# Optimization experiments

Hardware: AMD Instinct MI355X
Metric: run time of the kernel (lower is better)

The kernel has to match this reference:

```python
import jax, jax.numpy as jnp
import numpy as np

N_NODES = 50000
N_EDGES = 1600000
SLOPE = 0.01  # LeakyReLU default negative slope


def _leaky(x):
    return jnp.where(x >= 0, x, SLOPE * x)


def _gcn(x, W, b, row, col, num_nodes):
    """PyG GCNConv: x' = D^{-1/2}(A+I)D^{-1/2} X W + b (self-loops already in row/col)."""
    x = x @ W  # [N, 64]
    deg = jax.ops.segment_sum(jnp.ones_like(row, dtype=x.dtype), col, num_segments=num_nodes)
    dinv = jnp.where(deg > 0, jax.lax.rsqrt(deg), 0.0)
    norm = dinv[row] * dinv[col]  # [E+N]
    msg = x[row] * norm[:, None]  # gather + scale, [E+N, 64]
    out = jax.ops.segment_sum(msg, col, num_segments=num_nodes)
    return out + b


def setup_inputs() -> dict:
    key = jax.random.key(0)
    ks = jax.random.split(key, 24)
    d = {}
    d["screen"] = jax.random.normal(ks[0], (N_NODES, 768), jnp.float32)
    d["des"] = jax.random.normal(ks[1], (N_NODES, 768), jnp.float32)
    d["tweet"] = jax.random.normal(ks[2], (N_NODES, 768), jnp.float32)
    d["profile"] = jax.random.normal(ks[3], (N_NODES, 5), jnp.float32)
    d["personal"] = jax.random.normal(ks[4], (N_NODES, 7), jnp.float32)
    d["edge"] = jax.random.randint(ks[5], (2, N_EDGES), 0, N_NODES, dtype=jnp.int32)

    def lin(k, fan_in, fan_out):
        s = 1.0 / np.sqrt(fan_in)
        k1, k2 = jax.random.split(k)
        W = jax.random.uniform(k1, (fan_in, fan_out), jnp.float32, -s, s)
        b = jax.random.uniform(k2, (fan_out,), jnp.float32, -s, s)
        return W, b

    d["W_screen"], d["b_screen"] = lin(ks[6], 768, 16)
    d["W_des"], d["b_des"] = lin(ks[7], 768, 16)
    d["W_tweet"], d["b_tweet"] = lin(ks[8], 768, 16)
    d["W_pro"], d["b_pro"] = lin(ks[9], 5, 8)
    d["W_per"], d["b_per"] = lin(ks[10], 7, 8)
    d["W_lin"], d["b_lin"] = lin(ks[11], 64, 64)
    d["W_g1"], d["b_g1"] = lin(ks[12], 64, 64)
    d["W_g2"], d["b_g2"] = lin(ks[13], 64, 64)
    d["W_g3"], d["b_g3"] = lin(ks[14], 64, 64)
    d["W_o1"], d["b_o1"] = lin(ks[15], 64, 64)
    d["W_o2"], d["b_o2"] = lin(ks[16], 64, 2)
    return d


def reference(screen, des, tweet, profile, personal, edge,
              W_screen, b_screen, W_des, b_des, W_tweet, b_tweet,
              W_pro, b_pro, W_per, b_per, W_lin, b_lin,
              W_g1, b_g1, W_g2, b_g2, W_g3, b_g3,
              W_o1, b_o1, W_o2, b_o2):
    n = screen.shape[0]
    # dropout layers act as identity in eval mode
    s = _leaky(screen @ W_screen + b_screen)
    de = _leaky(des @ W_des + b_des)
    t = _leaky(tweet @ W_tweet + b_tweet)
    p = _leaky(profile @ W_pro + b_pro)
    pe = _leaky(personal @ W_per + b_per)
    x1 = jnp.concatenate((s, de, t, p, pe), axis=1)  # [N, 64]
    x = _leaky(x1 @ W_lin + b_lin)
    # add self-loops once (shared by all three GCN layers)
    loops = jnp.arange(n, dtype=edge.dtype)
    row = jnp.concatenate([edge[0], loops])
    col = jnp.concatenate([edge[1], loops])
    x = _gcn(x, W_g1, b_g1, row, col, n) + x1
    x = _gcn(x, W_g2, b_g2, row, col, n) + x1
    x = _gcn(x, W_g3, b_g3, row, col, n) + x1
    x = _leaky(x @ W_o1 + b_o1)
    return jax.nn.sigmoid(x @ W_o2 + b_o2)
```

## Files before the change

### kernel.cpp

```cpp
#include <hip/hip_runtime.h>

__device__ __forceinline__ float leaky(float v) { return v >= 0.f ? v : 0.01f * v; }

__device__ __forceinline__ void fma4(float4& a, float s, const float4& w) {
    a.x = fmaf(s, w.x, a.x); a.y = fmaf(s, w.y, a.y);
    a.z = fmaf(s, w.z, a.z); a.w = fmaf(s, w.w, a.w);
}

__device__ __forceinline__ unsigned short f2bf(float x) {
    unsigned b = __float_as_uint(x);
    return (unsigned short)((b + 0x7FFFu + ((b >> 16) & 1u)) >> 16);
}
__device__ __forceinline__ float bf2f(unsigned short u) {
    return __uint_as_float(((unsigned)u) << 16);
}

typedef __attribute__((ext_vector_type(8))) short short8v;
typedef __attribute__((ext_vector_type(4))) float float4v;

__global__ __launch_bounds__(256) void k_scan_part(const int* __restrict__ deg,
                                                   int* __restrict__ part,
                                                   int* __restrict__ bsum, int N) {
    __shared__ int tmp[256];
    int tid = threadIdx.x;
    int i = blockIdx.x * 256 + tid;
    int v = (i < N) ? deg[i] : 0;
    tmp[tid] = v;
    __syncthreads();
    for (int ofs = 1; ofs < 256; ofs <<= 1) {
        int t = (tid >= ofs) ? tmp[tid - ofs] : 0;
        __syncthreads();
        tmp[tid] += t;
        __syncthreads();
    }
    int incl = tmp[tid];
    if (i < N) part[i] = incl - v;
    if (tid == 255) bsum[blockIdx.x] = incl;
}

__global__ __launch_bounds__(256) void k_scan_sums(const int* __restrict__ bsum,
                                                   int* __restrict__ boff, int NB,
                                                   int* __restrict__ offs_last) {
    __shared__ int tmp[256];
    int tid = threadIdx.x;
    int v = (tid < NB) ? bsum[tid] : 0;
    tmp[tid] = v;
    __syncthreads();
    for (int ofs = 1; ofs < 256; ofs <<= 1) {
        int t = (tid >= ofs) ? tmp[tid - ofs] : 0;
        __syncthreads();
        tmp[tid] += t;
        __syncthreads();
    }
    int incl = tmp[tid];
    if (tid < NB) boff[tid] = incl - v;
    if (tid == 255) offs_last[0] = incl;
}

__global__ __launch_bounds__(256) void k_scan_final(const int* __restrict__ part,
                                                    const int* __restrict__ boff,
                                                    const int* __restrict__ deg,
                                                    int* __restrict__ offs,
                                                    int* __restrict__ pos,
                                                    float* __restrict__ dinv, int N) {
    int i = blockIdx.x * 256 + threadIdx.x;
    if (i < N) {
        int o = part[i] + boff[blockIdx.x];
        offs[i] = o;
        pos[i] = o;
        dinv[i] = rsqrtf((float)(deg[i] + 1));
    }
}

__global__ __launch_bounds__(512) void k_featB(
    const float* __restrict__ s, const float* __restrict__ d, const float* __restrict__ t,
    const float* __restrict__ Ws, const float* __restrict__ bs2,
    const float* __restrict__ Wd, const float* __restrict__ bd2,
    const float* __restrict__ Wt, const float* __restrict__ bt2,
    const float* __restrict__ prof, const float* __restrict__ pers,
    const float* __restrict__ Wp, const float* __restrict__ bp,
    const float* __restrict__ Wpe, const float* __restrict__ bpe,
    const int* __restrict__ colv, int* __restrict__ deg, int E,
    float* __restrict__ x1g, int N, int NG, int NSM) {
    __shared__ short8v wfv[3072];

    const int bid = blockIdx.x;
    const int tid = threadIdx.x;

    {
        const int NW = 3 * NG + NSM;
        int eper = (E + NW - 1) / NW;
        int ebase = bid * eper;
        int eend = ebase + eper; if (eend > E) eend = E;
        for (int e = ebase + tid; e < eend; e += 512)
            atomicAdd(&deg[colv[e]], 1);
    }

    if (bid >= 3 * NG) {
        int n = (bid - 3 * NG) * 512 + tid;
        if (n >= N) return;
        float pv[5], pe[7];
#pragma unroll
        for (int i = 0; i < 5; ++i) pv[i] = prof[(size_t)n * 5 + i];
#pragma unroll
        for (int i = 0; i < 7; ++i) pe[i] = pers[(size_t)n * 7 + i];
        float o[16];
#pragma unroll
        for (int j = 0; j < 8; ++j) {
            float a = bp[j];
#pragma unroll
            for (int i = 0; i < 5; ++i) a = fmaf(pv[i], Wp[i * 8 + j], a);
            o[j] = leaky(a);
            float a2 = bpe[j];
#pragma unroll
            for (int i = 0; i < 7; ++i) a2 = fmaf(pe[i], Wpe[i * 8 + j], a2);
            o[8 + j] = leaky(a2);
        }
#pragma unroll
        for (int v = 0; v < 4; ++v)
            *reinterpret_cast<float4*>(x1g + (size_t)n * 64 + 48 + v * 4) =
                make_float4(o[v * 4], o[v * 4 + 1], o[v * 4 + 2], o[v * 4 + 3]);
        return;
    }

    const int f = bid / NG;
    const int grp = bid - f * NG;
    const float* __restrict__ X = (f == 0) ? s : ((f == 1) ? d : t);
    const float* __restrict__ W = (f == 0) ? Ws : ((f == 1) ? Wd : Wt);
    const float* __restrict__ B = (f == 0) ? bs2 : ((f == 1) ? bd2 : bt2);
    const int n0 = grp * 128;
    const int lane = tid & 63;
    const int wid = tid >> 6;

    short* wfs = (short*)wfv;
#pragma unroll
    for (int v = 0; v < 6; ++v) {
        int idx4 = tid + v * 512;
        float4 w4 = *reinterpret_cast<const float4*>(W + (size_t)idx4 * 4);
        int k = idx4 >> 2;
        int j0 = (idx4 & 3) * 4;
        int c = k >> 5, g = (k >> 3) & 3, i = k & 7;
        float wq[4] = {w4.x, w4.y, w4.z, w4.w};
#pragma unroll
        for (int q = 0; q < 4; ++q) {
            int sl = (c * 64 + g * 16 + j0 + q) * 8 + i;
            unsigned short h = f2bf(wq[q]);
            wfs[sl] = (short)h;
            wfs[12288 + sl] = (short)f2bf(wq[q] - bf2f(h));
        }
    }
    __syncthreads();

    const int nb = n0 + wid * 16;
    int mrow = nb + (lane & 15); if (mrow >= N) mrow = N - 1;
    const float* base = X + (size_t)mrow * 768 + ((lane >> 4) << 3);

    float4 pa[4], pb[4];
#pragma unroll
    for (int u = 0; u < 4; ++u) {
        pa[u] = *reinterpret_cast<const float4*>(base + u * 32);
        pb[u] = *reinterpret_cast<const float4*>(base + u * 32 + 4);
    }
    __builtin_amdgcn_sched_barrier(0);
    float4v acc = {0.f, 0.f, 0.f, 0.f};

#pragma unroll
    for (int c = 0; c < 24; ++c) {
        const int u = c & 3;
        float xs[8] = {pa[u].x, pa[u].y, pa[u].z, pa[u].w,
                       pb[u].x, pb[u].y, pb[u].z, pb[u].w};
        if (c + 4 < 24) {
            pa[u] = *reinterpret_cast<const float4*>(base + (c + 4) * 32);
            pb[u] = *reinterpret_cast<const float4*>(base + (c + 4) * 32 + 4);
        }
        short8v xh, xl;
#pragma unroll
        for (int i = 0; i < 8; ++i) {
            unsigned short h = f2bf(xs[i]);
            xh[i] = (short)h;
            xl[i] = (short)f2bf(xs[i] - bf2f(h));
        }
        short8v wh = wfv[c * 64 + lane];
        short8v wl = wfv[1536 + c * 64 + lane];
        acc = __builtin_amdgcn_mfma_f32_16x16x32_bf16(xh, wh, acc, 0, 0, 0);
        acc = __builtin_amdgcn_mfma_f32_16x16x32_bf16(xl, wh, acc, 0, 0, 0);
        acc = __builtin_amdgcn_mfma_f32_16x16x32_bf16(xh, wl, acc, 0, 0, 0);
        __builtin_amdgcn_sched_barrier(0);
    }

    int j = lane & 15;
    float bb = B[j];
#pragma unroll
    for (int r = 0; r < 4; ++r) {
        int n = nb + ((lane >> 4) << 2) + r;
        if (n < N) x1g[(size_t)n * 64 + f * 16 + j] = leaky(acc[r] + bb);
    }
}

__global__ __launch_bounds__(256) void k_lin1(const float* __restrict__ x1,
                                              const float* __restrict__ Wl,
                                              const float* __restrict__ bl,
                                              const float* __restrict__ Wg1,
                                              const float* __restrict__ dinvv,
                                              const int* __restrict__ rowv,
                                              const int* __restrict__ colv,
                                              int* __restrict__ pos,
                                              int* __restrict__ csr, int E,
                                              unsigned short* __restrict__ z,
                                              int N, int NGB) {
    __shared__ float4 xt4[1024];
    __shared__ float4 wt4[1024];
    const int tid = threadIdx.x;
    const int bid = blockIdx.x;

    {
        int eper = (E + NGB - 1) / NGB;
        int ebase = bid * eper;
        int eend = ebase + eper; if (eend > E) eend = E;
        int cols[8], rows[8];
#pragma unroll
        for (int r = 0; r < 8; ++r) {
            int e = ebase + tid + r * 256;
            cols[r] = (e < eend) ? colv[e] : -1;
            rows[r] = (e < eend) ? rowv[e] : 0;
        }
        int ps[8];
#pragma unroll
        for (int r = 0; r < 8; ++r)
            if (cols[r] >= 0) ps[r] = atomicAdd(&pos[cols[r]], 1);
#pragma unroll
        for (int r = 0; r < 8; ++r)
            if (cols[r] >= 0) csr[ps[r]] = rows[r];
    }

    const int n0 = bid * 64;
    const int nq = tid & 15;
    const int jq = tid >> 4;

#pragma unroll
    for (int v = 0; v < 4; ++v) {
        int L = v * 256 + tid;
        int n = L >> 4, c4 = L & 15;
        int nn = n0 + n; if (nn >= N) nn = N - 1;
        xt4[n * 16 + (c4 ^ (n & 15))] = *reinterpret_cast<const float4*>(x1 + (size_t)nn * 64 + c4 * 4);
        wt4[L] = *reinterpret_cast<const float4*>(Wl + (size_t)L * 4);
    }
    __syncthreads();

    float4 acc[4];
#pragma unroll
    for (int g = 0; g < 4; ++g) acc[g] = make_float4(0.f, 0.f, 0.f, 0.f);
    for (int k = 0; k < 64; k += 4) {
        float4 w0 = wt4[(k + 0) * 16 + jq];
        float4 w1 = wt4[(k + 1) * 16 + jq];
        float4 w2 = wt4[(k + 2) * 16 + jq];
        float4 w3 = wt4[(k + 3) * 16 + jq];
        int k4 = k >> 2;
#pragma unroll
        for (int g = 0; g < 4; ++g) {
            int n = nq + (g << 4);
            float4 xv = xt4[n * 16 + (k4 ^ (n & 15))];
            fma4(acc[g], xv.x, w0);
            fma4(acc[g], xv.y, w1);
            fma4(acc[g], xv.z, w2);
            fma4(acc[g], xv.w, w3);
        }
    }
    float4 bb = *reinterpret_cast<const float4*>(bl + jq * 4);
    __syncthreads();

#pragma unroll
    for (int g = 0; g < 4; ++g) {
        int n = nq + (g << 4);
        float4 h;
        h.x = leaky(acc[g].x + bb.x);
        h.y = leaky(acc[g].y + bb.y);
        h.z = leaky(acc[g].z + bb.z);
        h.w = leaky(acc[g].w + bb.w);
        xt4[n * 16 + (jq ^ (n & 15))] = h;
    }
#pragma unroll
    for (int v = 0; v < 4; ++v) {
        int L = v * 256 + tid;
        wt4[L] = *reinterpret_cast<const float4*>(Wg1 + (size_t)L * 4);
    }
    __syncthreads();

#pragma unroll
    for (int g = 0; g < 4; ++g) acc[g] = make_float4(0.f, 0.f, 0.f, 0.f);
    for (int k = 0; k < 64; k += 4) {
        float4 w0 = wt4[(k + 0) * 16 + jq];
        float4 w1 = wt4[(k + 1) * 16 + jq];
        float4 w2 = wt4[(k + 2) * 16 + jq];
        float4 w3 = wt4[(k + 3) * 16 + jq];
        int k4 = k >> 2;
#pragma unroll
        for (int g = 0; g < 4; ++g) {
            int n = nq + (g << 4);
            float4 xv = xt4[n * 16 + (k4 ^ (n & 15))];
            fma4(acc[g], xv.x, w0);
            fma4(acc[g], xv.y, w1);
            fma4(acc[g], xv.z, w2);
            fma4(acc[g], xv.w, w3);
        }
    }
#pragma unroll
    for (int g = 0; g < 4; ++g) {
        int n = nq + (g << 4);
        if (n0 + n >= N) continue;
        float dv = dinvv[n0 + n];
        ushort4 o;
        o.x = f2bf(acc[g].x * dv); o.y = f2bf(acc[g].y * dv);
        o.z = f2bf(acc[g].z * dv); o.w = f2bf(acc[g].w * dv);
        *reinterpret_cast<ushort4*>(z + (size_t)(n0 + n) * 64 + jq * 4) = o;
    }
}

__global__ __launch_bounds__(256, 4) void k_mm64(const float* __restrict__ xin,
                                                 const float* __restrict__ W,
                                                 const float* __restrict__ dinvv,
                                                 unsigned short* __restrict__ z, int N) {
    __shared__ float4 xt4[1024];
    __shared__ float4 wt4[1024];
    const int tid = threadIdx.x;
    const int n0 = blockIdx.x * 64;
#pragma unroll
    for (int v = 0; v < 4; ++v) {
        int L = v * 256 + tid;
        int n = L >> 4, c4 = L & 15;
        int nn = n0 + n; if (nn >= N) nn = N - 1;
        xt4[n * 16 + (c4 ^ (n & 15))] = *reinterpret_cast<const float4*>(xin + (size_t)nn * 64 + c4 * 4);
        wt4[L] = *reinterpret_cast<const float4*>(W + (size_t)L * 4);
    }
    __syncthreads();
    const int nq = tid & 15;
    const int jq = tid >> 4;
    float4 acc[4];
#pragma unroll
    for (int g = 0; g < 4; ++g) acc[g] = make_float4(0.f, 0.f, 0.f, 0.f);
    for (int k = 0; k < 64; k += 4) {
        float4 w0 = wt4[(k + 0) * 16 + jq];
        float4 w1 = wt4[(k + 1) * 16 + jq];
        float4 w2 = wt4[(k + 2) * 16 + jq];
        float4 w3 = wt4[(k + 3) * 16 + jq];
        int k4 = k >> 2;
#pragma unroll
        for (int g = 0; g < 4; ++g) {
            int n = nq + (g << 4);
            float4 xv = xt4[n * 16 + (k4 ^ (n & 15))];
            fma4(acc[g], xv.x, w0);
            fma4(acc[g], xv.y, w1);
            fma4(acc[g], xv.z, w2);
            fma4(acc[g], xv.w, w3);
        }
    }
#pragma unroll
    for (int g = 0; g < 4; ++g) {
        int n = nq + (g << 4);
        if (n0 + n >= N) continue;
        float dv = dinvv[n0 + n];
        ushort4 o;
        o.x = f2bf(acc[g].x * dv); o.y = f2bf(acc[g].y * dv);
        o.z = f2bf(acc[g].z * dv); o.w = f2bf(acc[g].w * dv);
        *reinterpret_cast<ushort4*>(z + (size_t)(n0 + n) * 64 + jq * 4) = o;
    }
}

__global__ __launch_bounds__(256) void k_agg(const unsigned short* __restrict__ z,
                                             const int* __restrict__ offs,
                                             const int* __restrict__ csr,
                                             const float* __restrict__ dinv,
                                             const float* __restrict__ bias,
                                             const float* __restrict__ x1,
                                             float* __restrict__ xout, int N) {
    int lane = threadIdx.x & 63;
    int c = blockIdx.x * 4 + (threadIdx.x >> 6);
    if (c >= N) return;
    int s = __builtin_amdgcn_readfirstlane(offs[c]);
    int e = __builtin_amdgcn_readfirstlane(offs[c + 1]);
    const int half = lane >> 5;
    const int d = lane & 31;
    const unsigned* __restrict__ zr = (const unsigned*)z;

    float ax = 0.f, ay = 0.f;
    if (half == 0) {
        unsigned sv = zr[(size_t)c * 32 + d];
        ax = bf2f((unsigned short)(sv & 0xffffu));
        ay = bf2f((unsigned short)(sv >> 16));
    }
    float ux[8] = {0, 0, 0, 0, 0, 0, 0, 0};
    float uy[8] = {0, 0, 0, 0, 0, 0, 0, 0};
    int j = s;
    for (; j + 16 <= e; j += 16) {
#pragma unroll
        for (int u = 0; u < 8; ++u) {
            int r0 = csr[j + 2 * u];
            int r1 = csr[j + 2 * u + 1];
            int r = half ? r1 : r0;
            unsigned v = zr[(size_t)r * 32 + d];
            ux[u] += bf2f((unsigned short)(v & 0xffffu));
            uy[u] += bf2f((unsigned short)(v >> 16));
        }
    }
    for (; j + 2 <= e; j += 2) {
        int r0 = csr[j];
        int r1 = csr[j + 1];
        int r = half ? r1 : r0;
        unsigned v = zr[(size_t)r * 32 + d];
        ax += bf2f((unsigned short)(v & 0xffffu));
        ay += bf2f((unsigned short)(v >> 16));
    }
    if (j < e && half == 0) {
        int r = csr[j];
        unsigned v = zr[(size_t)r * 32 + d];
        ax += bf2f((unsigned short)(v & 0xffffu));
        ay += bf2f((unsigned short)(v >> 16));
    }
    float tx = ax + ((ux[0] + ux[1]) + (ux[2] + ux[3])) + ((ux[4] + ux[5]) + (ux[6] + ux[7]));
    float ty = ay + ((uy[0] + uy[1]) + (uy[2] + uy[3])) + ((uy[4] + uy[5]) + (uy[6] + uy[7]));
    tx += __shfl_xor(tx, 32);
    ty += __shfl_xor(ty, 32);
    if (half == 0) {
        float dv = dinv[c];
        float2 bb = reinterpret_cast<const float2*>(bias)[d];
        float2 xx = *reinterpret_cast<const float2*>(x1 + (size_t)c * 64 + 2 * d);
        float2 o;
        o.x = dv * tx + bb.x + xx.x;
        o.y = dv * ty + bb.y + xx.y;
        *reinterpret_cast<float2*>(xout + (size_t)c * 64 + 2 * d) = o;
    }
}

__global__ __launch_bounds__(256) void k_head(const float* __restrict__ xin,
                                              const float* __restrict__ Wo1,
                                              const float* __restrict__ bo1,
                                              const float* __restrict__ Wo2,
                                              const float* __restrict__ bo2,
                                              float* __restrict__ out, int N) {
    __shared__ float xsg[64][65];
    __shared__ float wg[64][65];
    __shared__ float hs[64][65];
    __shared__ float wo2[128];
    const int tid = threadIdx.x;
    const int n0 = blockIdx.x * 64;
#pragma unroll
    for (int v = 0; v < 4; ++v) {
        int idx = tid + v * 256;
        int n = idx >> 4;
        int jj = (idx & 15) << 2;
        float4 xv = make_float4(0.f, 0.f, 0.f, 0.f);
        if (n0 + n < N) xv = *reinterpret_cast<const float4*>(xin + (size_t)(n0 + n) * 64 + jj);
        xsg[n][jj] = xv.x; xsg[n][jj + 1] = xv.y; xsg[n][jj + 2] = xv.z; xsg[n][jj + 3] = xv.w;
        float4 w = *reinterpret_cast<const float4*>(Wo1 + (size_t)n * 64 + jj);
        wg[n][jj] = w.x; wg[n][jj + 1] = w.y; wg[n][jj + 2] = w.z; wg[n][jj + 3] = w.w;
    }
    if (tid < 128) wo2[tid] = Wo2[tid];
    __syncthreads();
    int j = tid & 63;
    int g = tid >> 6;
    float bj = bo1[j];
    for (int i = 0; i < 16; ++i) {
        int n = g * 16 + i;
        float a = bj;
#pragma unroll
        for (int k = 0; k < 64; ++k) a += xsg[n][k] * wg[k][j];
        hs[n][j] = leaky(a);
    }
    __syncthreads();
    if (tid < 128) {
        int n = tid >> 1;
        int j2 = tid & 1;
        float a = bo2[j2];
#pragma unroll
        for (int k = 0; k < 64; ++k) a += hs[n][k] * wo2[k * 2 + j2];
        if (n0 + n < N) out[(size_t)(n0 + n) * 2 + j2] = 1.f / (1.f + expf(-a));
    }
}

extern "C" void kernel_launch(void* const* d_in, const int* in_sizes, int n_in,
                              void* d_out, int out_size, void* d_ws, size_t ws_size,
                              hipStream_t stream) {
    const float* screen   = (const float*)d_in[0];
    const float* des      = (const float*)d_in[1];
    const float* tweet    = (const float*)d_in[2];
    const float* profile  = (const float*)d_in[3];
    const float* personal = (const float*)d_in[4];
    const int*   edge     = (const int*)d_in[5];
    const float* Ws  = (const float*)d_in[6],  *bs  = (const float*)d_in[7];
    const float* Wd  = (const float*)d_in[8],  *bd  = (const float*)d_in[9];
    const float* Wt  = (const float*)d_in[10], *bt  = (const float*)d_in[11];
    const float* Wp  = (const float*)d_in[12], *bp  = (const float*)d_in[13];
    const float* Wpe = (const float*)d_in[14], *bpe = (const float*)d_in[15];
    const float* Wl  = (const float*)d_in[16], *bl  = (const float*)d_in[17];
    const float* Wg1 = (const float*)d_in[18], *bg1 = (const float*)d_in[19];
    const float* Wg2 = (const float*)d_in[20], *bg2 = (const float*)d_in[21];
    const float* Wg3 = (const float*)d_in[22], *bg3 = (const float*)d_in[23];
    const float* Wo1 = (const float*)d_in[24], *bo1 = (const float*)d_in[25];
    const float* Wo2 = (const float*)d_in[26], *bo2 = (const float*)d_in[27];

    const int N = in_sizes[0] / 768;
    const int E = in_sizes[5] / 2;
    const int* row = edge;
    const int* col = edge + E;

    size_t off = 0;
    auto alloc = [&](size_t bytes) -> void* {
        void* p = (char*)d_ws + off;
        off += (bytes + 255) & ~(size_t)255;
        return p;
    };
    const size_t NF = (size_t)N * 64;
    float* x1   = (float*)alloc(NF * 4);
    float* xa   = (float*)alloc(NF * 4);
    float* xb   = (float*)alloc(NF * 4);
    unsigned short* z = (unsigned short*)alloc(NF * 2);
    float* dinv = (float*)alloc((size_t)N * 4);
    int* deg  = (int*)alloc((size_t)N * 4);
    int* part = (int*)alloc((size_t)N * 4);
    int* offs = (int*)alloc((size_t)(N + 1) * 4);
    int* pos  = (int*)alloc((size_t)N * 4);
    int* csr  = (int*)alloc((size_t)E * 4);
    const int NB = (N + 255) / 256;
    int* bsum = (int*)alloc((size_t)NB * 4);
    int* boff = (int*)alloc((size_t)NB * 4);
    (void)ws_size; (void)n_in; (void)out_size;

    hipMemsetAsync(deg, 0, (size_t)N * 4, stream);

    const int NG = (N + 127) / 128;
    const int NSM = (N + 511) / 512;
    k_featB<<<NG * 3 + NSM, 512, 0, stream>>>(screen, des, tweet,
                                              Ws, bs, Wd, bd, Wt, bt,
                                              profile, personal, Wp, bp, Wpe, bpe,
                                              col, deg, E,
                                              x1, N, NG, NSM);

    k_scan_part<<<NB, 256, 0, stream>>>(deg, part, bsum, N);
    k_scan_sums<<<1, 256, 0, stream>>>(bsum, boff, NB, offs + N);
    k_scan_final<<<NB, 256, 0, stream>>>(part, boff, deg, offs, pos, dinv, N);

    const int NGB = (N + 63) / 64;
    const int NAB = (N + 3) / 4;
    k_lin1<<<NGB, 256, 0, stream>>>(x1, Wl, bl, Wg1, dinv,
                                    row, col, pos, csr, E, z, N, NGB);
    k_agg<<<NAB, 256, 0, stream>>>(z, offs, csr, dinv, bg1, x1, xb, N);
    k_mm64<<<NGB, 256, 0, stream>>>(xb, Wg2, dinv, z, N);
    k_agg<<<NAB, 256, 0, stream>>>(z, offs, csr, dinv, bg2, x1, xa, N);
    k_mm64<<<NGB, 256, 0, stream>>>(xa, Wg3, dinv, z, N);
    k_agg<<<NAB, 256, 0, stream>>>(z, offs, csr, dinv, bg3, x1, xb, N);

    k_head<<<NGB, 256, 0, stream>>>(xb, Wo1, bo1, Wo2, bo2, (float*)d_out, N);
}
```

Before: 467.5 us.

## Fuse GCN aggregation with next layer matmul and output head

Merges the per-node aggregation kernel with the following 64x64 transform (producing the next bf16 z directly) and, for the last layer, with the two-layer output head. This removes the fp32 intermediate activation buffers, their global writes and reads, and two kernel launches. In exchange each 4-node block reloads the full 64x64 weight matrix into shared memory and adds a block barrier after the latency-bound gather phase.

Result: faster. 405.5 us (-13.3%).

```diff
diff --git a/kernel.cpp b/kernel.cpp
--- a/kernel.cpp
+++ b/kernel.cpp
@@ -316,164 +316,201 @@
     }
 }
 
-__global__ __launch_bounds__(256, 4) void k_mm64(const float* __restrict__ xin,
-                                                 const float* __restrict__ W,
-                                                 const float* __restrict__ dinvv,
-                                                 unsigned short* __restrict__ z, int N) {
-    __shared__ float4 xt4[1024];
+__global__ __launch_bounds__(256) void k_aggmm(const unsigned short* __restrict__ z,
+                                               const int* __restrict__ offs,
+                                               const int* __restrict__ csr,
+                                               const float* __restrict__ dinv,
+                                               const float* __restrict__ bias,
+                                               const float* __restrict__ x1,
+                                               const float* __restrict__ Wn,
+                                               unsigned short* __restrict__ zout,
+                                               int N) {
+    __shared__ float xs[4][68];
     __shared__ float4 wt4[1024];
     const int tid = threadIdx.x;
-    const int n0 = blockIdx.x * 64;
-#pragma unroll
-    for (int v = 0; v < 4; ++v) {
-        int L = v * 256 + tid;
-        int n = L >> 4, c4 = L & 15;
-        int nn = n0 + n; if (nn >= N) nn = N - 1;
-        xt4[n * 16 + (c4 ^ (n & 15))] = *reinterpret_cast<const float4*>(xin + (size_t)nn * 64 + c4 * 4);
-        wt4[L] = *reinterpret_cast<const float4*>(W + (size_t)L * 4);
-    }
-    __syncthreads();
-    const int nq = tid & 15;
-    const int jq = tid >> 4;
-    float4 acc[4];
-#pragma unroll
-    for (int g = 0; g < 4; ++g) acc[g] = make_float4(0.f, 0.f, 0.f, 0.f);
-    for (int k = 0; k < 64; k += 4) {
-        float4 w0 = wt4[(k + 0) * 16 + jq];
-        float4 w1 = wt4[(k + 1) * 16 + jq];
-        float4 w2 = wt4[(k + 2) * 16 + jq];
-        float4 w3 = wt4[(k + 3) * 16 + jq];
-        int k4 = k >> 2;
-#pragma unroll
-        for (int g = 0; g < 4; ++g) {
-            int n = nq + (g << 4);
-            float4 xv = xt4[n * 16 + (k4 ^ (n & 15))];
-            fma4(acc[g], xv.x, w0);
-            fma4(acc[g], xv.y, w1);
-            fma4(acc[g], xv.z, w2);
-            fma4(acc[g], xv.w, w3);
-        }
-    }
-#pragma unroll
-    for (int g = 0; g < 4; ++g) {
-        int n = nq + (g << 4);
-        if (n0 + n >= N) continue;
-        float dv = dinvv[n0 + n];
-        ushort4 o;
-        o.x = f2bf(acc[g].x * dv); o.y = f2bf(acc[g].y * dv);
-        o.z = f2bf(acc[g].z * dv); o.w = f2bf(acc[g].w * dv);
-        *reinterpret_cast<ushort4*>(z + (size_t)(n0 + n) * 64 + jq * 4) = o;
-    }
-}
-
-__global__ __launch_bounds__(256) void k_agg(const unsigned short* __restrict__ z,
-                                             const int* __restrict__ offs,
-                                             const int* __restrict__ csr,
-                                             const float* __restrict__ dinv,
-                                             const float* __restrict__ bias,
-                                             const float* __restrict__ x1,
-                                             float* __restrict__ xout, int N) {
-    int lane = threadIdx.x & 63;
-    int c = blockIdx.x * 4 + (threadIdx.x >> 6);
-    if (c >= N) return;
-    int s = __builtin_amdgcn_readfirstlane(offs[c]);
-    int e = __builtin_amdgcn_readfirstlane(offs[c + 1]);
-    const int half = lane >> 5;
-    const int d = lane & 31;
-    const unsigned* __restrict__ zr = (const unsigned*)z;
-
-    float ax = 0.f, ay = 0.f;
-    if (half == 0) {
-        unsigned sv = zr[(size_t)c * 32 + d];
-        ax = bf2f((unsigned short)(sv & 0xffffu));
-        ay = bf2f((unsigned short)(sv >> 16));
-    }
-    float ux[8] = {0, 0, 0, 0, 0, 0, 0, 0};
-    float uy[8] = {0, 0, 0, 0, 0, 0, 0, 0};
-    int j = s;
-    for (; j + 16 <= e; j += 16) {
-#pragma unroll
-        for (int u = 0; u < 8; ++u) {
-            int r0 = csr[j + 2 * u];
-            int r1 = csr[j + 2 * u + 1];
+    const int lane = tid & 63;
+    const int wid = tid >> 6;
+    const int c0 = blockIdx.x * 4;
+    const int c = c0 + wid;
+
+#pragma unroll
+    for (int v = 0; v < 4; ++v)
+        wt4[v * 256 + tid] = *reinterpret_cast<const float4*>(Wn + (size_t)(v * 256 + tid) * 4);
+
+    if (c < N) {
+        int s = __builtin_amdgcn_readfirstlane(offs[c]);
+        int e = __builtin_amdgcn_readfirstlane(offs[c + 1]);
+        const int half = lane >> 5;
+        const int d = lane & 31;
+        const unsigned* __restrict__ zr = (const unsigned*)z;
+
+        float ax = 0.f, ay = 0.f;
+        if (half == 0) {
+            unsigned sv = zr[(size_t)c * 32 + d];
+            ax = bf2f((unsigned short)(sv & 0xffffu));
+            ay = bf2f((unsigned short)(sv >> 16));
+        }
+        float ux[8] = {0, 0, 0, 0, 0, 0, 0, 0};
+        float uy[8] = {0, 0, 0, 0, 0, 0, 0, 0};
+        int j = s;
+        for (; j + 16 <= e; j += 16) {
+#pragma unroll
+            for (int u = 0; u < 8; ++u) {
+                int r0 = csr[j + 2 * u];
+                int r1 = csr[j + 2 * u + 1];
+                int r = half ? r1 : r0;
+                unsigned v = zr[(size_t)r * 32 + d];
+                ux[u] += bf2f((unsigned short)(v & 0xffffu));
+                uy[u] += bf2f((unsigned short)(v >> 16));
+            }
+        }
+        for (; j + 2 <= e; j += 2) {
+            int r0 = csr[j];
+            int r1 = csr[j + 1];
             int r = half ? r1 : r0;
             unsigned v = zr[(size_t)r * 32 + d];
-            ux[u] += bf2f((unsigned short)(v & 0xffffu));
-            uy[u] += bf2f((unsigned short)(v >> 16));
-        }
-    }
-    for (; j + 2 <= e; j += 2) {
-        int r0 = csr[j];
-        int r1 = csr[j + 1];
-        int r = half ? r1 : r0;
-        unsigned v = zr[(size_t)r * 32 + d];
-        ax += bf2f((unsigned short)(v & 0xffffu));
-        ay += bf2f((unsigned short)(v >> 16));
-    }
-    if (j < e && half == 0) {
-        int r = csr[j];
-        unsigned v = zr[(size_t)r * 32 + d];
-        ax += bf2f((unsigned short)(v & 0xffffu));
-        ay += bf2f((unsigned short)(v >> 16));
-    }
-    float tx = ax + ((ux[0] + ux[1]) + (ux[2] + ux[3])) + ((ux[4] + ux[5]) + (ux[6] + ux[7]));
-    float ty = ay + ((uy[0] + uy[1]) + (uy[2] + uy[3])) + ((uy[4] + uy[5]) + (uy[6] + uy[7]));
-    tx += __shfl_xor(tx, 32);
-    ty += __shfl_xor(ty, 32);
-    if (half == 0) {
-        float dv = dinv[c];
-        float2 bb = reinterpret_cast<const float2*>(bias)[d];
-        float2 xx = *reinterpret_cast<const float2*>(x1 + (size_t)c * 64 + 2 * d);
-        float2 o;
-        o.x = dv * tx + bb.x + xx.x;
-        o.y = dv * ty + bb.y + xx.y;
-        *reinterpret_cast<float2*>(xout + (size_t)c * 64 + 2 * d) = o;
-    }
-}
-
-__global__ __launch_bounds__(256) void k_head(const float* __restrict__ xin,
-                                              const float* __restrict__ Wo1,
-                                              const float* __restrict__ bo1,
-                                              const float* __restrict__ Wo2,
-                                              const float* __restrict__ bo2,
-                                              float* __restrict__ out, int N) {
-    __shared__ float xsg[64][65];
-    __shared__ float wg[64][65];
-    __shared__ float hs[64][65];
+            ax += bf2f((unsigned short)(v & 0xffffu));
+            ay += bf2f((unsigned short)(v >> 16));
+        }
+        if (j < e && half == 0) {
+            int r = csr[j];
+            unsigned v = zr[(size_t)r * 32 + d];
+            ax += bf2f((unsigned short)(v & 0xffffu));
+            ay += bf2f((unsigned short)(v >> 16));
+        }
+        float tx = ax + ((ux[0] + ux[1]) + (ux[2] + ux[3])) + ((ux[4] + ux[5]) + (ux[6] + ux[7]));
+        float ty = ay + ((uy[0] + uy[1]) + (uy[2] + uy[3])) + ((uy[4] + uy[5]) + (uy[6] + uy[7]));
+        tx += __shfl_xor(tx, 32);
+        ty += __shfl_xor(ty, 32);
+        if (half == 0) {
+            float dv = dinv[c];
+            float2 bb = reinterpret_cast<const float2*>(bias)[d];
+            float2 xx = *reinterpret_cast<const float2*>(x1 + (size_t)c * 64 + 2 * d);
+            xs[wid][2 * d] = dv * tx + bb.x + xx.x;
+            xs[wid][2 * d + 1] = dv * ty + bb.y + xx.y;
+        }
+    }
+    __syncthreads();
+
+    {
+        int n = wid;
+        int cn = c0 + n;
+        if (cn < N) {
+            const float* W = (const float*)wt4;
+            float y = 0.f;
+#pragma unroll
+            for (int k = 0; k < 64; ++k)
+                y = fmaf(xs[n][k], W[k * 64 + lane], y);
+            zout[(size_t)cn * 64 + lane] = f2bf(y * dinv[cn]);
+        }
+    }
+}
+
+__global__ __launch_bounds__(256) void k_agghead(const unsigned short* __restrict__ z,
+                                                 const int* __restrict__ offs,
+                                                 const int* __restrict__ csr,
+                                                 const float* __restrict__ dinv,
+                                                 const float* __restrict__ bias,
+                                                 const float* __restrict__ x1,
+                                                 const float* __restrict__ Wo1,
+                                                 const float* __restrict__ bo1,
+                                                 const float* __restrict__ Wo2,
+                                                 const float* __restrict__ bo2,
+                                                 float* __restrict__ out, int N) {
+    __shared__ float xs[4][68];
+    __shared__ float hs[4][68];
+    __shared__ float4 wt4[1024];
     __shared__ float wo2[128];
+    __shared__ float bo1s[64];
     const int tid = threadIdx.x;
-    const int n0 = blockIdx.x * 64;
-#pragma unroll
-    for (int v = 0; v < 4; ++v) {
-        int idx = tid + v * 256;
-        int n = idx >> 4;
-        int jj = (idx & 15) << 2;
-        float4 xv = make_float4(0.f, 0.f, 0.f, 0.f);
-        if (n0 + n < N) xv = *reinterpret_cast<const float4*>(xin + (size_t)(n0 + n) * 64 + jj);
-        xsg[n][jj] = xv.x; xsg[n][jj + 1] = xv.y; xsg[n][jj + 2] = xv.z; xsg[n][jj + 3] = xv.w;
-        float4 w = *reinterpret_cast<const float4*>(Wo1 + (size_t)n * 64 + jj);
-        wg[n][jj] = w.x; wg[n][jj + 1] = w.y; wg[n][jj + 2] = w.z; wg[n][jj + 3] = w.w;
-    }
+    const int lane = tid & 63;
+    const int wid = tid >> 6;
+    const int c0 = blockIdx.x * 4;
+    const int c = c0 + wid;
+
+#pragma unroll
+    for (int v = 0; v < 4; ++v)
+        wt4[v * 256 + tid] = *reinterpret_cast<const float4*>(Wo1 + (size_t)(v * 256 + tid) * 4);
     if (tid < 128) wo2[tid] = Wo2[tid];
-    __syncthreads();
-    int j = tid & 63;
-    int g = tid >> 6;
-    float bj = bo1[j];
-    for (int i = 0; i < 16; ++i) {
-        int n = g * 16 + i;
-        float a = bj;
-#pragma unroll
-        for (int k = 0; k < 64; ++k) a += xsg[n][k] * wg[k][j];
-        hs[n][j] = leaky(a);
-    }
-    __syncthreads();
-    if (tid < 128) {
+    if (tid < 64) bo1s[tid] = bo1[tid];
+
+    if (c < N) {
+        int s = __builtin_amdgcn_readfirstlane(offs[c]);
+        int e = __builtin_amdgcn_readfirstlane(offs[c + 1]);
+        const int half = lane >> 5;
+        const int d = lane & 31;
+        const unsigned* __restrict__ zr = (const unsigned*)z;
+
+        float ax = 0.f, ay = 0.f;
+        if (half == 0) {
+            unsigned sv = zr[(size_t)c * 32 + d];
+            ax = bf2f((unsigned short)(sv & 0xffffu));
+            ay = bf2f((unsigned short)(sv >> 16));
+        }
+        float ux[8] = {0, 0, 0, 0, 0, 0, 0, 0};
+        float uy[8] = {0, 0, 0, 0, 0, 0, 0, 0};
+        int j = s;
+        for (; j + 16 <= e; j += 16) {
+#pragma unroll
+            for (int u = 0; u < 8; ++u) {
+                int r0 = csr[j + 2 * u];
+                int r1 = csr[j + 2 * u + 1];
+                int r = half ? r1 : r0;
+                unsigned v = zr[(size_t)r * 32 + d];
+                ux[u] += bf2f((unsigned short)(v & 0xffffu));
+                uy[u] += bf2f((unsigned short)(v >> 16));
+            }
+        }
+        for (; j + 2 <= e; j += 2) {
+            int r0 = csr[j];
+            int r1 = csr[j + 1];
+            int r = half ? r1 : r0;
+            unsigned v = zr[(size_t)r * 32 + d];
+            ax += bf2f((unsigned short)(v & 0xffffu));
+            ay += bf2f((unsigned short)(v >> 16));
+        }
+        if (j < e && half == 0) {
+            int r = csr[j];
+            unsigned v = zr[(size_t)r * 32 + d];
+            ax += bf2f((unsigned short)(v & 0xffffu));
+            ay += bf2f((unsigned short)(v >> 16));
+        }
+        float tx = ax + ((ux[0] + ux[1]) + (ux[2] + ux[3])) + ((ux[4] + ux[5]) + (ux[6] + ux[7]));
+        float ty = ay + ((uy[0] + uy[1]) + (uy[2] + uy[3])) + ((uy[4] + uy[5]) + (uy[6] + uy[7]));
+        tx += __shfl_xor(tx, 32);
+        ty += __shfl_xor(ty, 32);
+        if (half == 0) {
+            float dv = dinv[c];
+            float2 bb = reinterpret_cast<const float2*>(bias)[d];
+            float2 xx = *reinterpret_cast<const float2*>(x1 + (size_t)c * 64 + 2 * d);
+            xs[wid][2 * d] = dv * tx + bb.x + xx.x;
+            xs[wid][2 * d + 1] = dv * ty + bb.y + xx.y;
+        }
+    }
+    __syncthreads();
+
+    {
+        int n = wid;
+        const float* W = (const float*)wt4;
+        float y = bo1s[lane];
+#pragma unroll
+        for (int k = 0; k < 64; ++k)
+            y = fmaf(xs[n][k], W[k * 64 + lane], y);
+        hs[n][lane] = leaky(y);
+    }
+    __syncthreads();
+
+    if (tid < 8) {
         int n = tid >> 1;
         int j2 = tid & 1;
-        float a = bo2[j2];
-#pragma unroll
-        for (int k = 0; k < 64; ++k) a += hs[n][k] * wo2[k * 2 + j2];
-        if (n0 + n < N) out[(size_t)(n0 + n) * 2 + j2] = 1.f / (1.f + expf(-a));
+        int cn = c0 + n;
+        if (cn < N) {
+            float a = bo2[j2];
+#pragma unroll
+            for (int k = 0; k < 64; ++k)
+                a = fmaf(hs[n][k], wo2[k * 2 + j2], a);
+            out[(size_t)cn * 2 + j2] = 1.f / (1.f + expf(-a));
+        }
     }
 }
 
@@ -511,9 +548,8 @@
     };
     const size_t NF = (size_t)N * 64;
     float* x1   = (float*)alloc(NF * 4);
-    float* xa   = (float*)alloc(NF * 4);
-    float* xb   = (float*)alloc(NF * 4);
-    unsigned short* z = (unsigned short*)alloc(NF * 2);
+    unsigned short* za = (unsigned short*)alloc(NF * 2);
+    unsigned short* zb = (unsigned short*)alloc(NF * 2);
     float* dinv = (float*)alloc((size_t)N * 4);
     int* deg  = (int*)alloc((size_t)N * 4);
     int* part = (int*)alloc((size_t)N * 4);
@@ -542,12 +578,9 @@
     const int NGB = (N + 63) / 64;
     const int NAB = (N + 3) / 4;
     k_lin1<<<NGB, 256, 0, stream>>>(x1, Wl, bl, Wg1, dinv,
-                                    row, col, pos, csr, E, z, N, NGB);
-    k_agg<<<NAB, 256, 0, stream>>>(z, offs, csr, dinv, bg1, x1, xb, N);
-    k_mm64<<<NGB, 256, 0, stream>>>(xb, Wg2, dinv, z, N);
-    k_agg<<<NAB, 256, 0, stream>>>(z, offs, csr, dinv, bg2, x1, xa, N);
-    k_mm64<<<NGB, 256, 0, stream>>>(xa, Wg3, dinv, z, N);
-    k_agg<<<NAB, 256, 0, stream>>>(z, offs, csr, dinv, bg3, x1, xb, N);
-
-    k_head<<<NGB, 256, 0, stream>>>(xb, Wo1, bo1, Wo2, bo2, (float*)d_out, N);
-}
+                                    row, col, pos, csr, E, za, N, NGB);
+    k_aggmm<<<NAB, 256, 0, stream>>>(za, offs, csr, dinv, bg1, x1, Wg2, zb, N);
+    k_aggmm<<<NAB, 256, 0, stream>>>(zb, offs, csr, dinv, bg2, x1, Wg3, za, N);
+    k_agghead<<<NAB, 256, 0, stream>>>(za, offs, csr, dinv, bg3, x1,
+                                       Wo1, bo1, Wo2, bo2, (float*)d_out, N);
+}
```
